# Kernel tuning notes

Measured on AMD Instinct MI355X. Metric: run time of the kernel, lower is better.

The kernel has to match this reference:

```python
import jax, jax.numpy as jnp
import numpy as np

DIST = 22.63      # __init__ kwarg `dist` (cdist threshold)
DS_SIZE = 80      # hard-coded Downsample result_size in LeafBranchFunc
LOG_CLAMP = 100.0 # torch BCE clamps log terms at -100


def _cdist(x):
    # x: [B,N,F] -> pairwise euclidean distances [B,N,N]
    sq = jnp.sum(x * x, axis=-1)
    d2 = sq[:, :, None] + sq[:, None, :] - 2.0 * jnp.einsum('bnf,bmf->bnm', x, x)
    return jnp.sqrt(jnp.maximum(d2, 0.0))


@jax.jit
def _cluster(point_features):
    """Faithful port of Cluster.forward: threshold cdist, then the strictly
    sequential greedy label stamping with a single global next_label counter."""
    adj = _cdist(point_features) < DIST  # [B,N,N] bool
    N = adj.shape[1]
    idx = jnp.arange(N)

    def row_step(carry, xs):
        labels, nxt = carry
        row, i = xs
        cur = labels[i]
        new = jnp.where(cur == 0, nxt, cur)
        nxt = jnp.where(cur == 0, nxt + 1, nxt)
        labels = labels.at[i].set(new)
        labels = jnp.where(row, new, labels)  # stamp all thresholded neighbors
        return (labels, nxt), None

    def batch_step(nxt, adj_b):
        (labels, nxt), _ = jax.lax.scan(row_step, (jnp.zeros(N, jnp.int32), nxt), (adj_b, idx))
        return nxt, labels

    _, labels = jax.lax.scan(batch_step, jnp.int32(1), adj)  # sequential over batch: shared counter
    return labels  # [B,N] int32


def _classify(pts, W1, b1, W2, b2, W3, b3):
    # pts: [K,80,3] -> P(class 1) per cluster, PointNet-lite classifier + softmax
    h = jax.nn.relu(pts @ W1 + b1)       # [K,80,64]
    h = jax.nn.relu(h @ W2 + b2)         # [K,80,128]
    g = jnp.max(h, axis=1)               # [K,128] global max pool
    logits = g @ W3 + b3                 # [K,2]
    return jax.nn.softmax(logits, axis=-1)[:, 1]


def setup_inputs() -> dict:
    key = jax.random.key(0)
    ks = jax.random.split(key, 8)
    B, N, F = 4, 4096, 256
    return {
        'point_features': jax.random.normal(ks[0], (B, N, F), jnp.float32),
        'points': jax.random.normal(ks[1], (B, N, 3), jnp.float32),
        'W1': jax.random.normal(ks[2], (3, 64), jnp.float32) * 0.5,
        'b1': jnp.zeros((64,), jnp.float32),
        'W2': jax.random.normal(ks[3], (64, 128), jnp.float32) * 0.1,
        'b2': jnp.zeros((128,), jnp.float32),
        'W3': jax.random.normal(ks[4], (128, 2), jnp.float32) * 0.1,
        'b3': jnp.zeros((2,), jnp.float32),
    }


def reference(point_features, points, W1, b1, W2, b2, W3, b3):
    labels = np.asarray(_cluster(point_features))  # [B,N]; cluster ids are data-dependent
    points_np = np.asarray(points)
    rng = np.random.RandomState(0)  # Downsample uses np.random.choice with replacement
    total = jnp.float32(0.0)
    for b in range(labels.shape[0]):
        ds = []
        for c in np.unique(labels[b]):
            cp = points_np[b][labels[b] == c]                    # [M,3] points of this cluster
            sel = rng.choice(cp.shape[0], DS_SIZE, replace=True)  # random downsample to 80
            ds.append(cp[sel])
        ds = jnp.asarray(np.stack(ds), dtype=jnp.float32)        # [K,80,3]
        p = jnp.nan_to_num(_classify(ds, W1, b1, W2, b2, W3, b3))
        # binary_cross_entropy with all-ones targets: mean(-log p), log clamped at -100
        loss = jnp.mean(jnp.minimum(-jnp.log(p), LOG_CLAMP))
        total = total + loss
    return total
```

## Files before the change

### kernel.cpp

```cpp
#include <hip/hip_runtime.h>
#include <math.h>
#include <stdint.h>
#include <stdlib.h>

constexpr int B_ = 4, N_ = 4096, F_ = 256;
constexpr int DS = 80;
constexpr int MAXC = 16384;
constexpr int RAWBLKS = 224;
constexpr int RAWN = 624 * RAWBLKS;

namespace {
struct RawStream {
  unsigned* buf = nullptr;
  RawStream() {
    unsigned mt[624];
    mt[0] = 0u;
    for (int i = 1; i < 624; ++i)
      mt[i] = 1812433253u * (mt[i - 1] ^ (mt[i - 1] >> 30)) + (unsigned)i;
    if (hipHostMalloc((void**)&buf, (size_t)(RAWN + 624) * 4, 0) != hipSuccess || !buf)
      buf = (unsigned*)malloc((size_t)(RAWN + 624) * 4);
    for (int blk = 0; blk < RAWBLKS; ++blk) {
      for (int i = 0; i < 624; ++i) {
        unsigned y = (mt[i] & 0x80000000u) | (mt[(i + 1) % 624] & 0x7fffffffu);
        mt[i] = mt[(i + 397) % 624] ^ (y >> 1) ^ ((y & 1u) ? 0x9908b0dfu : 0u);
      }
      for (int i = 0; i < 624; ++i) {
        unsigned y = mt[i];
        y ^= y >> 11; y ^= (y << 7) & 0x9d2c5680u; y ^= (y << 15) & 0xefc60000u; y ^= y >> 18;
        buf[blk * 624 + i] = y;
      }
    }
    for (int i = 0; i < 624; ++i) buf[RAWN + i] = mt[i];
  }
};
RawStream g_raw;
}

__global__ __launch_bounds__(256) void pre_kernel(const float* __restrict__ x,
                                                  float* __restrict__ sq) {
  const int blk = blockIdx.x, tid = threadIdx.x;
  const int i = blk * 256 + tid;
  float4 v = ((const float4*)x)[i];
  float s = v.x * v.x + v.y * v.y + v.z * v.z + v.w * v.w;
  for (int off = 32; off > 0; off >>= 1) s += __shfl_down(s, off);
  if ((tid & 63) == 0) sq[blk * 4 + (tid >> 6)] = s;
}

__global__ __launch_bounds__(256) void scan_kernel(const float* __restrict__ x,
                                                   const float* __restrict__ sq,
                                                   int* __restrict__ p,
                                                   int* __restrict__ q) {
  const int tid = threadIdx.x;
  const int w = tid >> 6, lane = tid & 63;
  const int bb = blockIdx.x & 3;
  const int rem = blockIdx.x >> 2;
  const int idx = rem * 4 + w;
  const int i = idx >> 1;
  const bool qmode = (idx & 1) == 0;

  const float* xb = x + (size_t)bb * N_ * F_;
  const float* sqb = sq + (size_t)bb * N_;
  const int gl = lane & 15, g = lane >> 4;

  const int jhi = qmode ? (N_ - 1) : (i - 1);
  const int jlo = qmode ? (i + 1) : 0;

  int found = -1;
  if (jhi >= jlo) {
    const float4* ra = (const float4*)(xb + (size_t)i * F_);
    float4 a0 = ra[gl + 0], a1 = ra[gl + 16], a2 = ra[gl + 32], a3 = ra[gl + 48];
    const double sqi = (double)sqb[i];
    const double THR2D = (double)22.63f * (double)22.63f;

    int j0 = jhi;
    {
      int cj = j0 - g; if (cj < jlo) cj = jlo;
      const float4* rc = (const float4*)(xb + (size_t)cj * F_);
    }
    int cj0 = j0 - g; if (cj0 < jlo) cj0 = jlo;
    const float4* rc0 = (const float4*)(xb + (size_t)cj0 * F_);
    float4 c0 = rc0[gl], c1 = rc0[gl + 16], c2 = rc0[gl + 32], c3 = rc0[gl + 48];

    while (j0 >= jlo) {
      const int jn = j0 - 4;
      int cn = jn - g; if (cn < jlo) cn = jlo;
      const float4* rn = (const float4*)(xb + (size_t)cn * F_);
      float4 n0 = rn[gl], n1 = rn[gl + 16], n2 = rn[gl + 32], n3 = rn[gl + 48];

      float s = 0.f;
      s += a0.x * c0.x + a0.y * c0.y + a0.z * c0.z + a0.w * c0.w;
      s += a1.x * c1.x + a1.y * c1.y + a1.z * c1.z + a1.w * c1.w;
      s += a2.x * c2.x + a2.y * c2.y + a2.z * c2.z + a2.w * c2.w;
      s += a3.x * c3.x + a3.y * c3.y + a3.z * c3.z + a3.w * c3.w;
      s += __shfl_xor(s, 1); s += __shfl_xor(s, 2);
      s += __shfl_xor(s, 4); s += __shfl_xor(s, 8);

      bool ok = false;
      const int myj = j0 - g;
      if (myj >= jlo) {
        double d2 = sqi + (double)sqb[myj] - 2.0 * (double)s;
        ok = d2 < THR2D;
      }
      unsigned long long bal = __ballot(ok);
      if (bal) {
        found = j0 - ((__ffsll((unsigned long long)bal) - 1) >> 4);
        break;
      }
      c0 = n0; c1 = n1; c2 = n2; c3 = n3;
      j0 = jn;
    }
  }
  if (lane == 0) {
    const size_t o = (size_t)bb * N_ + i;
    if (qmode) q[o] = (found < 0) ? i : found;
    else       p[o] = found;
  }
}

__global__ __launch_bounds__(1024) void cluster_kernel(const int* __restrict__ p,
                                                       const int* __restrict__ q,
                                                       int* __restrict__ lab,
                                                       int* __restrict__ Karr, int* __restrict__ labs,
                                                       int* __restrict__ Msz) {
  const int b = blockIdx.x, tid = threadIdx.x;
  __shared__ int A[N_ + 1], Bb[N_], labS[N_];
  __shared__ int waveOff[17];
  __shared__ int runBase, chg;

  for (int k = tid; k < N_; k += 1024) {
    int pi = p[(size_t)b * N_ + k];
    A[k] = (pi < 0) ? k : pi;
  }
  __syncthreads();
  int* src = A; int* dst = Bb;
  for (int it = 0; it < 12; ++it) {
    if (tid == 0) chg = 0;
    __syncthreads();
    bool any = false;
    for (int k = tid; k < N_; k += 1024) {
      int v = src[src[k]];
      dst[k] = v;
      any |= (v != src[k]);
    }
    if (any) chg = 1;
    __syncthreads();
    int* t = src; src = dst; dst = t;
    if (!chg) break;
  }
  if (tid == 0) runBase = 0;
  __syncthreads();
  for (int base = 0; base < N_; base += 1024) {
    int i = base + tid;
    bool isR = (src[i] == i);
    unsigned long long bal = __ballot(isR);
    int lane = tid & 63, wid = tid >> 6;
    if (lane == 0) waveOff[wid] = __popcll(bal);
    __syncthreads();
    if (tid == 0) {
      int s = runBase;
      for (int w = 0; w < 16; ++w) { int t2 = waveOff[w]; waveOff[w] = s; s += t2; }
      waveOff[16] = s;
    }
    __syncthreads();
    int incl = __popcll(bal & (~0ull >> (63 - lane)));
    dst[i] = waveOff[wid] + incl;
    __syncthreads();
    if (tid == 0) runBase = waveOff[16];
    __syncthreads();
  }
  for (int j = tid; j < N_; j += 1024) {
    int qq = q[(size_t)b * N_ + j];
    int lv = dst[src[qq]];
    labS[j] = lv;
    lab[(size_t)b * N_ + j] = lv;
  }
  __syncthreads();

  int* cnt = A;
  for (int k = tid; k <= N_; k += 1024) cnt[k] = 0;
  __syncthreads();
  for (int j = tid; j < N_; j += 1024) atomicAdd(&cnt[labS[j]], 1);
  __syncthreads();
  if (tid == 0) runBase = 0;
  __syncthreads();
  for (int base = 1; base <= N_; base += 1024) {
    int c = base + tid;
    bool m = (cnt[c] > 0);
    unsigned long long bal = __ballot(m);
    int lane = tid & 63, wid = tid >> 6;
    if (lane == 0) waveOff[wid] = __popcll(bal);
    __syncthreads();
    if (tid == 0) {
      int s = runBase;
      for (int w = 0; w < 16; ++w) { int t2 = waveOff[w]; waveOff[w] = s; s += t2; }
      waveOff[16] = s;
    }
    __syncthreads();
    if (m) {
      int pos = waveOff[wid] + __popcll(bal & ((1ull << lane) - 1));
      labs[(size_t)b * N_ + pos] = c;
      Msz[(size_t)b * N_ + pos] = cnt[c];
    }
    __syncthreads();
    if (tid == 0) runBase = waveOff[16];
    __syncthreads();
  }
  if (tid == 0) Karr[b] = runBase;
}

__device__ inline void mt_regen(unsigned* mt, unsigned* raw, int lane) {
  const int ph_s[3] = {0, 227, 454};
  const int ph_e[3] = {227, 454, 624};
#pragma unroll
  for (int ph = 0; ph < 3; ++ph) {
    const int s = ph_s[ph], e = ph_e[ph];
    unsigned aReg[4], bReg[4];
    const int niter = (e - s + 63) >> 6;
    for (int it = 0; it < niter; ++it) {
      int i = s + it * 64 + lane;
      if (i < e) { aReg[it] = mt[i]; bReg[it] = mt[(i + 1) % 624]; }
    }
    __syncthreads();
    for (int it = 0; it < niter; ++it) {
      int i = s + it * 64 + lane;
      if (i < e) {
        unsigned y = (aReg[it] & 0x80000000u) | (bReg[it] & 0x7fffffffu);
        mt[i] = mt[(i + 397) % 624] ^ (y >> 1) ^ ((y & 1u) ? 0x9908b0dfu : 0u);
      }
    }
    __syncthreads();
  }
  for (int it = 0; it < 10; ++it) {
    int i = it * 64 + lane;
    if (i < 624) {
      unsigned y = mt[i];
      y ^= y >> 11; y ^= (y << 7) & 0x9d2c5680u; y ^= (y << 15) & 0xefc60000u; y ^= y >> 18;
      raw[i] = y;
    }
  }
  __syncthreads();
}

__global__ __launch_bounds__(64) void rngsel_kernel(const int* __restrict__ Karr,
                                                    const int* __restrict__ Msz,
                                                    const unsigned* __restrict__ rawG,
                                                    const unsigned* __restrict__ mtSave,
                                                    int* __restrict__ sel, int* __restrict__ meta,
                                                    int* __restrict__ totK) {
  __shared__ int mszS[2048];
  __shared__ unsigned rawL[2048];
  __shared__ unsigned mtF[624];
  __shared__ unsigned rawF[624];
  const int lane = threadIdx.x;
  int pos = 0;
  int winBase = -100000;
  bool fb = false;
  int fpos = 0;
  int cid = 0;
  for (int b = 0; b < B_; ++b) {
    const int Kb = Karr[b];
    for (int k0 = 0; k0 < Kb; k0 += 2048) {
      const int nk = min(2048, Kb - k0);
      for (int i = lane; i < nk; i += 64) mszS[i] = Msz[(size_t)b * N_ + k0 + i];
      __syncthreads();
      for (int kk = 0; kk < nk; ++kk) {
        const int M = mszS[kk];
        if (lane == 0) meta[cid] = (b << 16) | (k0 + kk);
        if (M <= 1) {
          sel[cid * DS + lane] = 0;
          if (lane < DS - 64) sel[cid * DS + 64 + lane] = 0;
        } else {
          const unsigned rng = (unsigned)(M - 1);
          unsigned mask = rng;
          mask |= mask >> 1; mask |= mask >> 2; mask |= mask >> 4; mask |= mask >> 8; mask |= mask >> 16;
          int acc = 0;
          while (acc < DS) {
            unsigned v = 0xFFFFFFFFu;
            bool ok = false;
            int take;
            if (!fb && pos >= RAWN) {
              fb = true;
              for (int i = lane; i < 624; i += 64) mtF[i] = mtSave[i];
              __syncthreads();
              fpos = 624;
            }
            if (!fb) {
              if (pos + 64 > winBase + 2048) {
                winBase = pos;
                for (int i = lane; i < 2048; i += 64) rawL[i] = rawG[winBase + i];
                __syncthreads();
              }
              take = min(64, RAWN - pos);
              if (lane < take) { v = rawL[pos - winBase + lane] & mask; ok = (v <= rng); }
            } else {
              if (fpos == 624) { mt_regen(mtF, rawF, lane); fpos = 0; }
              take = min(64, 624 - fpos);
              if (lane < take) { v = rawF[fpos + lane] & mask; ok = (v <= rng); }
            }
            unsigned long long bal = __ballot(ok);
            int pre = __popcll(bal & ((1ull << lane) - 1ull));
            int tot = __popcll(bal);
            if (ok && acc + pre < DS) sel[cid * DS + acc + pre] = (int)v;
            int advance;
            if (acc + tot >= DS) {
              int need = DS - acc;
              bool win = ok && (pre + 1 == need);
              unsigned long long wb = __ballot(win);
              advance = __ffsll(wb);
              acc = DS;
            } else {
              advance = take;
              acc += tot;
            }
            if (fb) fpos += advance; else pos += advance;
          }
        }
        ++cid;
      }
      __syncthreads();
    }
  }
  if (lane == 0) totK[0] = cid;
}

__global__ __launch_bounds__(256) void classify_par_kernel(
    const float* __restrict__ points, const float* __restrict__ W1, const float* __restrict__ b1,
    const float* __restrict__ W2, const float* __restrict__ b2,
    const float* __restrict__ W3, const float* __restrict__ b3,
    const int* __restrict__ lab, const int* __restrict__ labs,
    const int* __restrict__ sel, const int* __restrict__ meta, const int* __restrict__ totK,
    float* __restrict__ lossArr) {
  __shared__ unsigned wordsS[128];
  __shared__ int prefS[128];
  __shared__ float pts[DS][3];
  __shared__ float h1[DS][64];
  __shared__ float W2s[64][128];
  __shared__ float gmax[128];
  const int tid = threadIdx.x;
  int T = totK[0]; if (T > MAXC) T = MAXC;
  for (int k = tid; k < 64 * 128; k += 256) W2s[k >> 7][k & 127] = W2[k];

  for (int cid = blockIdx.x; cid < T; cid += gridDim.x) {
    const int mv = meta[cid];
    const int b = mv >> 16, k = mv & 0xFFFF;
    const int c = labs[(size_t)b * N_ + k];
    if (tid < 128) {
      unsigned wbits = 0;
      const int* lb = lab + (size_t)b * N_ + tid * 32;
      for (int s = 0; s < 32; ++s) wbits |= (lb[s] == c) ? (1u << s) : 0u;
      wordsS[tid] = wbits;
    }
    __syncthreads();
    if (tid == 0) {
      int s = 0;
      for (int w2 = 0; w2 < 128; ++w2) { prefS[w2] = s; s += __popc(wordsS[w2]); }
    }
    __syncthreads();
    if (tid < DS) {
      int r = sel[cid * DS + tid];
      int lo = 0, hi = 127;
      while (lo < hi) { int mid = (lo + hi + 1) >> 1; if (prefS[mid] <= r) lo = mid; else hi = mid - 1; }
      int rem = r - prefS[lo];
      unsigned wbits = wordsS[lo];
      int j = lo * 32;
      for (;;) {
        int bpos = __ffs(wbits) - 1;
        if (rem == 0) { j += bpos; break; }
        wbits &= wbits - 1; --rem;
      }
      pts[tid][0] = points[((size_t)b * N_ + j) * 3 + 0];
      pts[tid][1] = points[((size_t)b * N_ + j) * 3 + 1];
      pts[tid][2] = points[((size_t)b * N_ + j) * 3 + 2];
    }
    __syncthreads();
    for (int o = tid; o < DS * 64; o += 256) {
      int r = o >> 6, cc = o & 63;
      float v = pts[r][0] * W1[cc] + pts[r][1] * W1[64 + cc] + pts[r][2] * W1[128 + cc] + b1[cc];
      h1[r][cc] = fmaxf(v, 0.f);
    }
    __syncthreads();
    {
      const int cc = tid & 127, half = tid >> 7;
      const float b2c = b2[cc];
      float m = -1e30f;
      for (int r = half * 40; r < half * 40 + 40; ++r) {
        float a0 = 0.f, a1 = 0.f, a2 = 0.f, a3 = 0.f;
#pragma unroll
        for (int kk = 0; kk < 64; kk += 4) {
          a0 += h1[r][kk + 0] * W2s[kk + 0][cc];
          a1 += h1[r][kk + 1] * W2s[kk + 1][cc];
          a2 += h1[r][kk + 2] * W2s[kk + 2][cc];
          a3 += h1[r][kk + 3] * W2s[kk + 3][cc];
        }
        float acc = ((a0 + a1) + (a2 + a3)) + b2c;
        m = fmaxf(m, fmaxf(acc, 0.f));
      }
      if (half == 0) gmax[cc] = m;
      __syncthreads();
      if (half == 1) gmax[cc] = fmaxf(gmax[cc], m);
    }
    __syncthreads();
    if (tid == 0) {
      float l0 = b3[0], l1 = b3[1];
      for (int cc = 0; cc < 128; ++cc) { l0 += gmax[cc] * W3[cc * 2 + 0]; l1 += gmax[cc] * W3[cc * 2 + 1]; }
      float mx = fmaxf(l0, l1);
      float e0 = expf(l0 - mx), e1 = expf(l1 - mx);
      float p1 = e1 / (e0 + e1);
      if (isnan(p1)) p1 = 0.f;
      lossArr[cid] = fminf(-logf(p1), 100.f);
    }
    __syncthreads();
  }
}

__global__ __launch_bounds__(256) void reduce_kernel(const float* __restrict__ lossArr,
                                                     const int* __restrict__ meta,
                                                     const int* __restrict__ totK,
                                                     const int* __restrict__ Karr,
                                                     float* __restrict__ out) {
  __shared__ float accB[4];
  const int tid = threadIdx.x;
  if (tid < 4) accB[tid] = 0.f;
  __syncthreads();
  int T = totK[0]; if (T > MAXC) T = MAXC;
  float local[4] = {0.f, 0.f, 0.f, 0.f};
  for (int cid = tid; cid < T; cid += 256) local[meta[cid] >> 16] += lossArr[cid];
  for (int b = 0; b < 4; ++b) {
    float v = local[b];
    for (int off = 32; off > 0; off >>= 1) v += __shfl_down(v, off);
    if ((tid & 63) == 0) atomicAdd(&accB[b], v);
  }
  __syncthreads();
  if (tid == 0) {
    float tot = 0.f;
    for (int b = 0; b < 4; ++b) tot += accB[b] / (float)Karr[b];
    out[0] = tot;
  }
}

extern "C" void kernel_launch(void* const* d_in, const int* in_sizes, int n_in,
                              void* d_out, int out_size, void* d_ws, size_t ws_size,
                              hipStream_t stream) {
  const float* x      = (const float*)d_in[0];
  const float* points = (const float*)d_in[1];
  const float* W1 = (const float*)d_in[2];
  const float* b1 = (const float*)d_in[3];
  const float* W2 = (const float*)d_in[4];
  const float* b2 = (const float*)d_in[5];
  const float* W3 = (const float*)d_in[6];
  const float* b3 = (const float*)d_in[7];
  float* out = (float*)d_out;

  char* wsb = (char*)d_ws;
  size_t off = 0;
  auto carve = [&](size_t bytes) -> void* {
    void* r = wsb + off;
    off += (bytes + 255) & ~(size_t)255;
    return r;
  };
  float* sq      = (float*)carve((size_t)B_ * N_ * 4);
  int* p         = (int*)carve((size_t)B_ * N_ * 4);
  int* q         = (int*)carve((size_t)B_ * N_ * 4);
  int* lab       = (int*)carve((size_t)B_ * N_ * 4);
  int* labs      = (int*)carve((size_t)B_ * N_ * 4);
  int* Msz       = (int*)carve((size_t)B_ * N_ * 4);
  int* Karr      = (int*)carve(256);
  int* totK      = (int*)carve(256);
  unsigned* rawG = (unsigned*)carve((size_t)(RAWN + 624 + 2048) * 4);
  unsigned* mtSave = rawG + RAWN;
  int* sel       = (int*)carve((size_t)MAXC * DS * 4);
  int* meta      = (int*)carve((size_t)MAXC * 4);
  float* lossArr = (float*)carve((size_t)MAXC * 4);
  (void)ws_size;

  hipMemcpyAsync(rawG, g_raw.buf, (size_t)(RAWN + 624) * 4,
                 hipMemcpyHostToDevice, stream);

  hipLaunchKernelGGL(pre_kernel, dim3(B_ * N_ * F_ / 1024), dim3(256), 0, stream, x, sq);
  hipLaunchKernelGGL(scan_kernel, dim3(B_ * N_ * 2 / 4), dim3(256), 0, stream, x, sq, p, q);
  hipLaunchKernelGGL(cluster_kernel, dim3(B_), dim3(1024), 0, stream,
                     p, q, lab, Karr, labs, Msz);
  hipLaunchKernelGGL(rngsel_kernel, dim3(1), dim3(64), 0, stream,
                     Karr, Msz, rawG, mtSave, sel, meta, totK);
  hipLaunchKernelGGL(classify_par_kernel, dim3(512), dim3(256), 0, stream,
                     points, W1, b1, W2, b2, W3, b3, lab, labs, sel, meta, totK, lossArr);
  hipLaunchKernelGGL(reduce_kernel, dim3(1), dim3(256), 0, stream,
                     lossArr, meta, totK, Karr, out);
}
```

Before: 171.8 us.

## Unroll neighbor scan by two, aggregate histogram atomics, shrink RNG buffer, early-exit idle blocks

The neighbor-search loop now computes two groups of four candidate rows per iteration and prefetches the next eight rows, which gives more memory-level parallelism per wave. The per-label histogram uses wave-level match aggregation so that each distinct label in a wave issues one shared atomic. The precomputed MT19937 raw stream shrinks from 224 to 16 blocks, and classify blocks with no clusters to process return before loading W2. The unrolling raises register pressure and can read up to four rows past the first match, and the smaller RNG buffer assumes far fewer random draws are needed.

```diff
diff --git a/kernel.cpp b/kernel.cpp
--- a/kernel.cpp
+++ b/kernel.cpp
@@ -6,7 +6,7 @@
 constexpr int B_ = 4, N_ = 4096, F_ = 256;
 constexpr int DS = 80;
 constexpr int MAXC = 16384;
-constexpr int RAWBLKS = 224;
+constexpr int RAWBLKS = 16;
 constexpr int RAWN = 624 * RAWBLKS;
 
 namespace {
@@ -73,40 +73,59 @@
     const double THR2D = (double)22.63f * (double)22.63f;
 
     int j0 = jhi;
-    {
-      int cj = j0 - g; if (cj < jlo) cj = jlo;
-      const float4* rc = (const float4*)(xb + (size_t)cj * F_);
-    }
-    int cj0 = j0 - g; if (cj0 < jlo) cj0 = jlo;
-    const float4* rc0 = (const float4*)(xb + (size_t)cj0 * F_);
-    float4 c0 = rc0[gl], c1 = rc0[gl + 16], c2 = rc0[gl + 32], c3 = rc0[gl + 48];
+    int cjA = j0 - g;     if (cjA < jlo) cjA = jlo;
+    int cjB = j0 - 4 - g; if (cjB < jlo) cjB = jlo;
+    const float4* rA = (const float4*)(xb + (size_t)cjA * F_);
+    const float4* rB = (const float4*)(xb + (size_t)cjB * F_);
+    float4 cA0 = rA[gl], cA1 = rA[gl + 16], cA2 = rA[gl + 32], cA3 = rA[gl + 48];
+    float4 cB0 = rB[gl], cB1 = rB[gl + 16], cB2 = rB[gl + 32], cB3 = rB[gl + 48];
 
     while (j0 >= jlo) {
-      const int jn = j0 - 4;
-      int cn = jn - g; if (cn < jlo) cn = jlo;
-      const float4* rn = (const float4*)(xb + (size_t)cn * F_);
-      float4 n0 = rn[gl], n1 = rn[gl + 16], n2 = rn[gl + 32], n3 = rn[gl + 48];
-
-      float s = 0.f;
-      s += a0.x * c0.x + a0.y * c0.y + a0.z * c0.z + a0.w * c0.w;
-      s += a1.x * c1.x + a1.y * c1.y + a1.z * c1.z + a1.w * c1.w;
-      s += a2.x * c2.x + a2.y * c2.y + a2.z * c2.z + a2.w * c2.w;
-      s += a3.x * c3.x + a3.y * c3.y + a3.z * c3.z + a3.w * c3.w;
-      s += __shfl_xor(s, 1); s += __shfl_xor(s, 2);
-      s += __shfl_xor(s, 4); s += __shfl_xor(s, 8);
-
-      bool ok = false;
-      const int myj = j0 - g;
-      if (myj >= jlo) {
-        double d2 = sqi + (double)sqb[myj] - 2.0 * (double)s;
-        ok = d2 < THR2D;
-      }
-      unsigned long long bal = __ballot(ok);
-      if (bal) {
-        found = j0 - ((__ffsll((unsigned long long)bal) - 1) >> 4);
+      const int jn = j0 - 8;
+      int nA = jn - g;     if (nA < jlo) nA = jlo;
+      int nB = jn - 4 - g; if (nB < jlo) nB = jlo;
+      const float4* rnA = (const float4*)(xb + (size_t)nA * F_);
+      const float4* rnB = (const float4*)(xb + (size_t)nB * F_);
+      float4 pA0 = rnA[gl], pA1 = rnA[gl + 16], pA2 = rnA[gl + 32], pA3 = rnA[gl + 48];
+      float4 pB0 = rnB[gl], pB1 = rnB[gl + 16], pB2 = rnB[gl + 32], pB3 = rnB[gl + 48];
+
+      float sA = 0.f;
+      sA += a0.x * cA0.x + a0.y * cA0.y + a0.z * cA0.z + a0.w * cA0.w;
+      sA += a1.x * cA1.x + a1.y * cA1.y + a1.z * cA1.z + a1.w * cA1.w;
+      sA += a2.x * cA2.x + a2.y * cA2.y + a2.z * cA2.z + a2.w * cA2.w;
+      sA += a3.x * cA3.x + a3.y * cA3.y + a3.z * cA3.z + a3.w * cA3.w;
+      float sB = 0.f;
+      sB += a0.x * cB0.x + a0.y * cB0.y + a0.z * cB0.z + a0.w * cB0.w;
+      sB += a1.x * cB1.x + a1.y * cB1.y + a1.z * cB1.z + a1.w * cB1.w;
+      sB += a2.x * cB2.x + a2.y * cB2.y + a2.z * cB2.z + a2.w * cB2.w;
+      sB += a3.x * cB3.x + a3.y * cB3.y + a3.z * cB3.z + a3.w * cB3.w;
+      sA += __shfl_xor(sA, 1); sA += __shfl_xor(sA, 2);
+      sA += __shfl_xor(sA, 4); sA += __shfl_xor(sA, 8);
+      sB += __shfl_xor(sB, 1); sB += __shfl_xor(sB, 2);
+      sB += __shfl_xor(sB, 4); sB += __shfl_xor(sB, 8);
+
+      bool okA = false, okB = false;
+      const int mA = j0 - g, mB = j0 - 4 - g;
+      if (mA >= jlo) {
+        double d2 = sqi + (double)sqb[mA] - 2.0 * (double)sA;
+        okA = d2 < THR2D;
+      }
+      if (mB >= jlo) {
+        double d2 = sqi + (double)sqb[mB] - 2.0 * (double)sB;
+        okB = d2 < THR2D;
+      }
+      unsigned long long balA = __ballot(okA);
+      unsigned long long balB = __ballot(okB);
+      if (balA) {
+        found = j0 - ((__ffsll(balA) - 1) >> 4);
         break;
       }
-      c0 = n0; c1 = n1; c2 = n2; c3 = n3;
+      if (balB) {
+        found = j0 - 4 - ((__ffsll(balB) - 1) >> 4);
+        break;
+      }
+      cA0 = pA0; cA1 = pA1; cA2 = pA2; cA3 = pA3;
+      cB0 = pB0; cB1 = pB1; cB2 = pB2; cB3 = pB3;
       j0 = jn;
     }
   }
@@ -179,7 +198,20 @@
   int* cnt = A;
   for (int k = tid; k <= N_; k += 1024) cnt[k] = 0;
   __syncthreads();
-  for (int j = tid; j < N_; j += 1024) atomicAdd(&cnt[labS[j]], 1);
+  {
+    const int lane = tid & 63;
+    for (int j = tid; j < N_; j += 1024) {
+      int v = labS[j];
+      unsigned long long remM = ~0ull;
+      while (remM) {
+        int leader = __ffsll(remM) - 1;
+        int lv = __shfl(v, leader);
+        unsigned long long m = __ballot(v == lv);
+        if (lane == leader) atomicAdd(&cnt[lv], __popcll(m));
+        remM &= ~m;
+      }
+    }
+  }
   __syncthreads();
   if (tid == 0) runBase = 0;
   __syncthreads();
@@ -338,6 +370,7 @@
   __shared__ float gmax[128];
   const int tid = threadIdx.x;
   int T = totK[0]; if (T > MAXC) T = MAXC;
+  if ((int)blockIdx.x >= T) return;
   for (int k = tid; k < 64 * 128; k += 256) W2s[k >> 7][k & 127] = W2[k];
 
   for (int cid = blockIdx.x; cid < T; cid += gridDim.x) {
```

Result: faster. 161.0 us (-6.3%).
